# Performance work log

Measured on AMD Instinct MI355X. Metric: run time of the kernel, lower is better.

The kernel has to match this reference:

```python
import jax, jax.numpy as jnp
import numpy as np

F, V, NF, T = 240, 100000, 16, 2048


def _mesh_normalize(v):
    # v: (B, N, 3)
    mmax = jnp.max(v, axis=1, keepdims=True)
    mmin = jnp.min(v, axis=1, keepdims=True)
    v = v - (mmax + mmin) / 2
    big = jnp.max(v.reshape(v.shape[0], -1), axis=1)
    return v / big[:, None, None]


def _qmult(q1, q0):
    # Hamilton product, matches the torch qmult coefficient layout (wxyz)
    w0, x0, y0, z0 = q0[..., 0], q0[..., 1], q0[..., 2], q0[..., 3]
    w1, x1, y1, z1 = q1[..., 0], q1[..., 1], q1[..., 2], q1[..., 3]
    return jnp.stack([
        -x1 * x0 - y1 * y0 - z1 * z0 + w1 * w0,
         x1 * w0 + y1 * z0 - z1 * y0 + w1 * x0,
        -x1 * z0 + y1 * w0 + z1 * x0 + w1 * y0,
         x1 * y0 - y1 * x0 + z1 * w0 + w1 * z0], axis=-1)


def setup_inputs() -> dict:
    key = jax.random.key(0)
    k1, k2, k3, k4, k5 = jax.random.split(key, 5)
    # parameters initialized as in __init__ plus small perturbation (as after some training)
    tr = jnp.zeros((1, 1, F, 3)).at[0, 0, 0, 2].set(2.0) + 0.01 * jax.random.normal(k1, (1, 1, F, 3))
    q = jnp.zeros((1, F, 4)).at[:, :, 0].set(1.0) + 0.01 * jax.random.normal(k2, (1, F, 4))
    vp = 0.01 * jax.random.normal(k3, (1, V, 3))
    tex = jnp.ones((1, NF, T, T)) + 0.1 * jax.random.normal(k4, (1, NF, T, T))
    iv = _mesh_normalize(jax.random.normal(k5, (1, V, 3)))
    off = jnp.zeros((1, 1, F, 7)).at[:, :, :, 3].set(1.0)  # identity quaternion offsets, zero translation offsets
    of = jnp.arange(F, dtype=jnp.int32)
    return dict(translation_p=tr, quaternion_p=q, vertices_p=vp, texture_map=tex,
                ivertices=iv, offsets=off, opt_frames=of)


def reference(translation_p, quaternion_p, vertices_p, texture_map, ivertices, offsets, opt_frames):
    # opt_frames == arange(F): every frame is optimized, so no detach branch fires
    # and the per-frame python loop vectorizes (no cross-frame data dependence in outputs).
    qf = quaternion_p[0]                                      # (F, 4)
    qn = qf / jnp.linalg.norm(qf, axis=-1, keepdims=True)
    offq = offsets[0, 0, :, 3:]                               # (F, 4)
    offn = offq / jnp.linalg.norm(offq, axis=-1, keepdims=True)
    qprod = _qmult(qn, offn)                                  # (F, 4)
    # frame 0 uses the bare normalized quaternion; frames >=1 include the offset product
    q_all = jnp.concatenate([qn[:1], qprod[1:]], axis=0)      # (F, 4)
    t_all = jnp.concatenate(
        [translation_p[:, :, :1], translation_p[:, :, 1:] + offsets[:, :, 1:, :3]], axis=2)  # (1,1,F,3)

    of = opt_frames
    w = (of - jnp.concatenate([of[:1], of[:-1]])).astype(t_all.dtype)  # (K,)

    # tdiff = wghts * comp_tran_diff(translation[0,0,opt_frames])
    t = t_all[0, 0][of]                                       # (K, 3)
    vd = jnp.abs(t[1:] - t[:-1])
    vd = jnp.where(vd < 0.2, jnp.zeros_like(vd), vd)
    vd = jnp.concatenate([jnp.zeros_like(vd[:1]), vd], axis=0)
    tdiff = w * jnp.linalg.norm(vd, axis=1)

    # qdiff: first entry is qdist(quaternion0, quaternion0) with quaternion0 = last-loop value
    qlast = q_all[-1]
    d0 = 1.0 - jnp.sum(qlast * qlast) ** 2
    qa = q_all[of[1:] - 1]
    qb = q_all[of[1:]]
    kd = 1.0 - jnp.sum(qa * qb, axis=-1) ** 2
    qdiff = w * jnp.concatenate([d0[None], kd], axis=0)

    # predict_vertices=True, mesh_normalize=True
    vertices = _mesh_normalize(ivertices + vertices_p)

    # features == 'deep' -> raw texture map (no sigmoid)
    return (t_all[:, :, of], q_all[None][:, of], vertices, texture_map, tdiff, qdiff)
```

## Files before the change

kernel.cpp:

```cpp
#include <hip/hip_runtime.h>
#include <float.h>
#include <math.h>

#define F_MAX 512
#define RED_BLOCKS 32
#define COPY_GRID 1024

typedef float f4 __attribute__((ext_vector_type(4)));

__global__ __launch_bounds__(256) void minmax_frames_kernel(
    const f4* __restrict__ iv4, const f4* __restrict__ vp4, int nv4,
    float* __restrict__ partial,
    const float* __restrict__ tr,
    const float* __restrict__ q,
    const float* __restrict__ off,
    const int*   __restrict__ of,
    float* __restrict__ out_t,
    float* __restrict__ out_q,
    float* __restrict__ out_td,
    float* __restrict__ out_qd,
    int F)
{
    const int t = threadIdx.x;

    if (blockIdx.x != 0) {
        float mx0=-FLT_MAX, mx1=-FLT_MAX, mx2=-FLT_MAX;
        float mn0= FLT_MAX, mn1= FLT_MAX, mn2= FLT_MAX;
        const int gstride = (gridDim.x - 1) * blockDim.x;
        for (int i = (blockIdx.x - 1) * blockDim.x + t; i < nv4; i += gstride) {
            f4 a = iv4[i] + vp4[i];
            switch (i % 3) {
            case 0:
                mx0=fmaxf(mx0,a[0]); mn0=fminf(mn0,a[0]);
                mx1=fmaxf(mx1,a[1]); mn1=fminf(mn1,a[1]);
                mx2=fmaxf(mx2,a[2]); mn2=fminf(mn2,a[2]);
                mx0=fmaxf(mx0,a[3]); mn0=fminf(mn0,a[3]);
                break;
            case 1:
                mx1=fmaxf(mx1,a[0]); mn1=fminf(mn1,a[0]);
                mx2=fmaxf(mx2,a[1]); mn2=fminf(mn2,a[1]);
                mx0=fmaxf(mx0,a[2]); mn0=fminf(mn0,a[2]);
                mx1=fmaxf(mx1,a[3]); mn1=fminf(mn1,a[3]);
                break;
            default:
                mx2=fmaxf(mx2,a[0]); mn2=fminf(mn2,a[0]);
                mx0=fmaxf(mx0,a[1]); mn0=fminf(mn0,a[1]);
                mx1=fmaxf(mx1,a[2]); mn1=fminf(mn1,a[2]);
                mx2=fmaxf(mx2,a[3]); mn2=fminf(mn2,a[3]);
                break;
            }
        }
        __shared__ float s[256][6];
        s[t][0]=mx0; s[t][1]=mx1; s[t][2]=mx2; s[t][3]=mn0; s[t][4]=mn1; s[t][5]=mn2;
        __syncthreads();
        for (int w = 128; w >= 1; w >>= 1) {
            if (t < w) {
                s[t][0] = fmaxf(s[t][0], s[t+w][0]);
                s[t][1] = fmaxf(s[t][1], s[t+w][1]);
                s[t][2] = fmaxf(s[t][2], s[t+w][2]);
                s[t][3] = fminf(s[t][3], s[t+w][3]);
                s[t][4] = fminf(s[t][4], s[t+w][4]);
                s[t][5] = fminf(s[t][5], s[t+w][5]);
            }
            __syncthreads();
        }
        if (t == 0) {
            #pragma unroll
            for (int k = 0; k < 6; ++k)
                partial[(blockIdx.x - 1)*6 + k] = s[0][k];
        }
        return;
    }

    __shared__ float qall[F_MAX][4];
    __shared__ float tall[F_MAX][3];

    for (int f = t; f < F; f += blockDim.x) {
        float w1 = q[4*f+0], x1 = q[4*f+1], y1 = q[4*f+2], z1 = q[4*f+3];
        float n1 = sqrtf(w1*w1 + x1*x1 + y1*y1 + z1*z1);
        w1 /= n1; x1 /= n1; y1 /= n1; z1 /= n1;
        float w0 = off[7*f+3], x0 = off[7*f+4], y0 = off[7*f+5], z0 = off[7*f+6];
        float n0 = sqrtf(w0*w0 + x0*x0 + y0*y0 + z0*z0);
        w0 /= n0; x0 /= n0; y0 /= n0; z0 /= n0;
        float pw = -x1*x0 - y1*y0 - z1*z0 + w1*w0;
        float px =  x1*w0 + y1*z0 - z1*y0 + w1*x0;
        float py = -x1*z0 + y1*w0 + z1*x0 + w1*y0;
        float pz =  x1*y0 - y1*x0 + z1*w0 + w1*z0;
        if (f == 0) { pw = w1; px = x1; py = y1; pz = z1; }
        qall[f][0] = pw; qall[f][1] = px; qall[f][2] = py; qall[f][3] = pz;
        float o0 = 0.f, o1 = 0.f, o2 = 0.f;
        if (f >= 1) { o0 = off[7*f+0]; o1 = off[7*f+1]; o2 = off[7*f+2]; }
        tall[f][0] = tr[3*f+0] + o0;
        tall[f][1] = tr[3*f+1] + o1;
        tall[f][2] = tr[3*f+2] + o2;
    }
    __syncthreads();

    for (int j = t; j < F; j += blockDim.x) {
        const int fj = of[j];
        out_t[3*j+0] = tall[fj][0];
        out_t[3*j+1] = tall[fj][1];
        out_t[3*j+2] = tall[fj][2];
        out_q[4*j+0] = qall[fj][0];
        out_q[4*j+1] = qall[fj][1];
        out_q[4*j+2] = qall[fj][2];
        out_q[4*j+3] = qall[fj][3];

        float wj = (j == 0) ? 0.0f : (float)(of[j] - of[j-1]);

        float td = 0.0f;
        if (j >= 1) {
            const int fp = of[j-1];
            float ssum = 0.0f;
            #pragma unroll
            for (int c = 0; c < 3; ++c) {
                float d = fabsf(tall[fj][c] - tall[fp][c]);
                if (d < 0.2f) d = 0.0f;
                ssum += d * d;
            }
            td = wj * sqrtf(ssum);
        }
        out_td[j] = td;

        float qd;
        if (j == 0) {
            float sm = qall[F-1][0]*qall[F-1][0] + qall[F-1][1]*qall[F-1][1]
                     + qall[F-1][2]*qall[F-1][2] + qall[F-1][3]*qall[F-1][3];
            qd = wj * (1.0f - sm*sm);
        } else {
            int ia = fj - 1;
            if (ia < 0) ia += F;
            float sm = qall[ia][0]*qall[fj][0] + qall[ia][1]*qall[fj][1]
                     + qall[ia][2]*qall[fj][2] + qall[ia][3]*qall[fj][3];
            qd = wj * (1.0f - sm*sm);
        }
        out_qd[j] = qd;
    }
}

__global__ __launch_bounds__(256) void copy_finalize_norm_kernel(
    const f4* __restrict__ tex, f4* __restrict__ out_tex, long n_tex4,
    const float* __restrict__ partial,
    const f4* __restrict__ iv4, const f4* __restrict__ vp4,
    f4* __restrict__ out_v, int nv4)
{
    const int t = threadIdx.x;
    const long nthreads = (long)gridDim.x * blockDim.x;

    for (long i = (long)blockIdx.x * blockDim.x + t; i < n_tex4; i += nthreads) {
        f4 v = __builtin_nontemporal_load(&tex[i]);
        out_tex[i] = v;
    }

    const int gvid = blockIdx.x * blockDim.x + t;
    if (gvid < nv4) {
        float mx0=-FLT_MAX, mx1=-FLT_MAX, mx2=-FLT_MAX;
        float mn0= FLT_MAX, mn1= FLT_MAX, mn2= FLT_MAX;
        #pragma unroll
        for (int b = 0; b < RED_BLOCKS; ++b) {
            mx0 = fmaxf(mx0, partial[6*b+0]);
            mx1 = fmaxf(mx1, partial[6*b+1]);
            mx2 = fmaxf(mx2, partial[6*b+2]);
            mn0 = fminf(mn0, partial[6*b+3]);
            mn1 = fminf(mn1, partial[6*b+4]);
            mn2 = fminf(mn2, partial[6*b+5]);
        }
        const float c0 = (mx0 + mn0) * 0.5f;
        const float c1 = (mx1 + mn1) * 0.5f;
        const float c2 = (mx2 + mn2) * 0.5f;
        const float big = fmaxf(fmaxf(mx0 - c0, mx1 - c1), mx2 - c2);

        f4 a = iv4[gvid] + vp4[gvid];
        f4 r;
        switch (gvid % 3) {
        case 0:
            r[0]=(a[0]-c0)/big; r[1]=(a[1]-c1)/big;
            r[2]=(a[2]-c2)/big; r[3]=(a[3]-c0)/big; break;
        case 1:
            r[0]=(a[0]-c1)/big; r[1]=(a[1]-c2)/big;
            r[2]=(a[2]-c0)/big; r[3]=(a[3]-c1)/big; break;
        default:
            r[0]=(a[0]-c2)/big; r[1]=(a[1]-c0)/big;
            r[2]=(a[2]-c1)/big; r[3]=(a[3]-c2)/big; break;
        }
        out_v[gvid] = r;
    }
}

extern "C" void kernel_launch(void* const* d_in, const int* in_sizes, int n_in,
                              void* d_out, int out_size, void* d_ws, size_t ws_size,
                              hipStream_t stream) {
    const float* tr  = (const float*)d_in[0];
    const float* q   = (const float*)d_in[1];
    const float* vp  = (const float*)d_in[2];
    const float* tex = (const float*)d_in[3];
    const float* iv  = (const float*)d_in[4];
    const float* off = (const float*)d_in[5];
    const int*   of  = (const int*)d_in[6];

    const int F    = in_sizes[6];
    const int nt   = in_sizes[0];
    const int nq   = in_sizes[1];
    const int nv   = in_sizes[2];
    const int ntex = in_sizes[3];

    float* out     = (float*)d_out;
    float* out_t   = out;
    float* out_q   = out + nt;
    float* out_v   = out + nt + nq;
    float* out_tex = out + nt + nq + nv;
    float* out_td  = out + (size_t)nt + nq + nv + ntex;
    float* out_qd  = out_td + F;

    float* partial = (float*)d_ws;

    const int nv4 = nv / 4;

    minmax_frames_kernel<<<RED_BLOCKS + 1, 256, 0, stream>>>(
        (const f4*)iv, (const f4*)vp, nv4, partial,
        tr, q, off, of, out_t, out_q, out_td, out_qd, F);

    const long n_tex4 = (long)ntex / 4;
    copy_finalize_norm_kernel<<<COPY_GRID, 256, 0, stream>>>(
        (const f4*)tex, (f4*)out_tex, n_tex4,
        partial, (const f4*)iv, (const f4*)vp, (f4*)out_v, nv4);
}
```

Measured before the change: 90.45 us.

## Fuse reduction and copy kernels into one launch with atomic flag handoff

Merges the min/max reduction kernel and the texture-copy/normalize kernel into a single launch. Blocks 1..32 publish partial reductions and bump a global counter with release semantics. The blocks that normalize vertices spin on that counter after finishing their texture copy. This removes one kernel launch and the serialization gap between them, but adds a memset and a spin-wait that depends on the reducer blocks being co-resident, which carries a deadlock risk if they are not scheduled.

```diff
diff --git a/kernel.cpp b/kernel.cpp
--- a/kernel.cpp
+++ b/kernel.cpp
@@ -8,9 +8,10 @@
 
 typedef float f4 __attribute__((ext_vector_type(4)));
 
-__global__ __launch_bounds__(256) void minmax_frames_kernel(
+__global__ __launch_bounds__(256) void fused_kernel(
+    const f4* __restrict__ tex, f4* __restrict__ out_tex, long n_tex4,
     const f4* __restrict__ iv4, const f4* __restrict__ vp4, int nv4,
-    float* __restrict__ partial,
+    float* __restrict__ partial, unsigned int* __restrict__ flag,
     const float* __restrict__ tr,
     const float* __restrict__ q,
     const float* __restrict__ off,
@@ -19,15 +20,17 @@
     float* __restrict__ out_q,
     float* __restrict__ out_td,
     float* __restrict__ out_qd,
+    f4* __restrict__ out_v,
     int F)
 {
     const int t = threadIdx.x;
-
-    if (blockIdx.x != 0) {
+    const int b = blockIdx.x;
+
+    if (b >= 1 && b <= RED_BLOCKS) {
         float mx0=-FLT_MAX, mx1=-FLT_MAX, mx2=-FLT_MAX;
         float mn0= FLT_MAX, mn1= FLT_MAX, mn2= FLT_MAX;
-        const int gstride = (gridDim.x - 1) * blockDim.x;
-        for (int i = (blockIdx.x - 1) * blockDim.x + t; i < nv4; i += gstride) {
+        const int gstride = RED_BLOCKS * 256;
+        for (int i = (b - 1) * 256 + t; i < nv4; i += gstride) {
             f4 a = iv4[i] + vp4[i];
             switch (i % 3) {
             case 0:
@@ -66,104 +69,98 @@
         }
         if (t == 0) {
             #pragma unroll
-            for (int k = 0; k < 6; ++k)
-                partial[(blockIdx.x - 1)*6 + k] = s[0][k];
-        }
-        return;
+            for (int k = 0; k < 6; ++k) partial[(b - 1)*6 + k] = s[0][k];
+            __hip_atomic_fetch_add(flag, 1u, __ATOMIC_RELEASE,
+                                   __HIP_MEMORY_SCOPE_AGENT);
+        }
+    } else if (b == 0) {
+        __shared__ float qall[F_MAX][4];
+        __shared__ float tall[F_MAX][3];
+
+        for (int f = t; f < F; f += blockDim.x) {
+            float w1 = q[4*f+0], x1 = q[4*f+1], y1 = q[4*f+2], z1 = q[4*f+3];
+            float n1 = sqrtf(w1*w1 + x1*x1 + y1*y1 + z1*z1);
+            w1 /= n1; x1 /= n1; y1 /= n1; z1 /= n1;
+            float w0 = off[7*f+3], x0 = off[7*f+4], y0 = off[7*f+5], z0 = off[7*f+6];
+            float n0 = sqrtf(w0*w0 + x0*x0 + y0*y0 + z0*z0);
+            w0 /= n0; x0 /= n0; y0 /= n0; z0 /= n0;
+            float pw = -x1*x0 - y1*y0 - z1*z0 + w1*w0;
+            float px =  x1*w0 + y1*z0 - z1*y0 + w1*x0;
+            float py = -x1*z0 + y1*w0 + z1*x0 + w1*y0;
+            float pz =  x1*y0 - y1*x0 + z1*w0 + w1*z0;
+            if (f == 0) { pw = w1; px = x1; py = y1; pz = z1; }
+            qall[f][0] = pw; qall[f][1] = px; qall[f][2] = py; qall[f][3] = pz;
+            float o0 = 0.f, o1 = 0.f, o2 = 0.f;
+            if (f >= 1) { o0 = off[7*f+0]; o1 = off[7*f+1]; o2 = off[7*f+2]; }
+            tall[f][0] = tr[3*f+0] + o0;
+            tall[f][1] = tr[3*f+1] + o1;
+            tall[f][2] = tr[3*f+2] + o2;
+        }
+        __syncthreads();
+
+        for (int j = t; j < F; j += blockDim.x) {
+            const int fj = of[j];
+            out_t[3*j+0] = tall[fj][0];
+            out_t[3*j+1] = tall[fj][1];
+            out_t[3*j+2] = tall[fj][2];
+            out_q[4*j+0] = qall[fj][0];
+            out_q[4*j+1] = qall[fj][1];
+            out_q[4*j+2] = qall[fj][2];
+            out_q[4*j+3] = qall[fj][3];
+
+            float wj = (j == 0) ? 0.0f : (float)(of[j] - of[j-1]);
+
+            float td = 0.0f;
+            if (j >= 1) {
+                const int fp = of[j-1];
+                float ssum = 0.0f;
+                #pragma unroll
+                for (int c = 0; c < 3; ++c) {
+                    float d = fabsf(tall[fj][c] - tall[fp][c]);
+                    if (d < 0.2f) d = 0.0f;
+                    ssum += d * d;
+                }
+                td = wj * sqrtf(ssum);
+            }
+            out_td[j] = td;
+
+            float qd;
+            if (j == 0) {
+                float sm = qall[F-1][0]*qall[F-1][0] + qall[F-1][1]*qall[F-1][1]
+                         + qall[F-1][2]*qall[F-1][2] + qall[F-1][3]*qall[F-1][3];
+                qd = wj * (1.0f - sm*sm);
+            } else {
+                int ia = fj - 1;
+                if (ia < 0) ia += F;
+                float sm = qall[ia][0]*qall[fj][0] + qall[ia][1]*qall[fj][1]
+                         + qall[ia][2]*qall[fj][2] + qall[ia][3]*qall[fj][3];
+                qd = wj * (1.0f - sm*sm);
+            }
+            out_qd[j] = qd;
+        }
     }
 
-    __shared__ float qall[F_MAX][4];
-    __shared__ float tall[F_MAX][3];
-
-    for (int f = t; f < F; f += blockDim.x) {
-        float w1 = q[4*f+0], x1 = q[4*f+1], y1 = q[4*f+2], z1 = q[4*f+3];
-        float n1 = sqrtf(w1*w1 + x1*x1 + y1*y1 + z1*z1);
-        w1 /= n1; x1 /= n1; y1 /= n1; z1 /= n1;
-        float w0 = off[7*f+3], x0 = off[7*f+4], y0 = off[7*f+5], z0 = off[7*f+6];
-        float n0 = sqrtf(w0*w0 + x0*x0 + y0*y0 + z0*z0);
-        w0 /= n0; x0 /= n0; y0 /= n0; z0 /= n0;
-        float pw = -x1*x0 - y1*y0 - z1*z0 + w1*w0;
-        float px =  x1*w0 + y1*z0 - z1*y0 + w1*x0;
-        float py = -x1*z0 + y1*w0 + z1*x0 + w1*y0;
-        float pz =  x1*y0 - y1*x0 + z1*w0 + w1*z0;
-        if (f == 0) { pw = w1; px = x1; py = y1; pz = z1; }
-        qall[f][0] = pw; qall[f][1] = px; qall[f][2] = py; qall[f][3] = pz;
-        float o0 = 0.f, o1 = 0.f, o2 = 0.f;
-        if (f >= 1) { o0 = off[7*f+0]; o1 = off[7*f+1]; o2 = off[7*f+2]; }
-        tall[f][0] = tr[3*f+0] + o0;
-        tall[f][1] = tr[3*f+1] + o1;
-        tall[f][2] = tr[3*f+2] + o2;
-    }
-    __syncthreads();
-
-    for (int j = t; j < F; j += blockDim.x) {
-        const int fj = of[j];
-        out_t[3*j+0] = tall[fj][0];
-        out_t[3*j+1] = tall[fj][1];
-        out_t[3*j+2] = tall[fj][2];
-        out_q[4*j+0] = qall[fj][0];
-        out_q[4*j+1] = qall[fj][1];
-        out_q[4*j+2] = qall[fj][2];
-        out_q[4*j+3] = qall[fj][3];
-
-        float wj = (j == 0) ? 0.0f : (float)(of[j] - of[j-1]);
-
-        float td = 0.0f;
-        if (j >= 1) {
-            const int fp = of[j-1];
-            float ssum = 0.0f;
-            #pragma unroll
-            for (int c = 0; c < 3; ++c) {
-                float d = fabsf(tall[fj][c] - tall[fp][c]);
-                if (d < 0.2f) d = 0.0f;
-                ssum += d * d;
-            }
-            td = wj * sqrtf(ssum);
-        }
-        out_td[j] = td;
-
-        float qd;
-        if (j == 0) {
-            float sm = qall[F-1][0]*qall[F-1][0] + qall[F-1][1]*qall[F-1][1]
-                     + qall[F-1][2]*qall[F-1][2] + qall[F-1][3]*qall[F-1][3];
-            qd = wj * (1.0f - sm*sm);
-        } else {
-            int ia = fj - 1;
-            if (ia < 0) ia += F;
-            float sm = qall[ia][0]*qall[fj][0] + qall[ia][1]*qall[fj][1]
-                     + qall[ia][2]*qall[fj][2] + qall[ia][3]*qall[fj][3];
-            qd = wj * (1.0f - sm*sm);
-        }
-        out_qd[j] = qd;
-    }
-}
-
-__global__ __launch_bounds__(256) void copy_finalize_norm_kernel(
-    const f4* __restrict__ tex, f4* __restrict__ out_tex, long n_tex4,
-    const float* __restrict__ partial,
-    const f4* __restrict__ iv4, const f4* __restrict__ vp4,
-    f4* __restrict__ out_v, int nv4)
-{
-    const int t = threadIdx.x;
     const long nthreads = (long)gridDim.x * blockDim.x;
-
-    for (long i = (long)blockIdx.x * blockDim.x + t; i < n_tex4; i += nthreads) {
+    for (long i = (long)b * blockDim.x + t; i < n_tex4; i += nthreads) {
         f4 v = __builtin_nontemporal_load(&tex[i]);
         out_tex[i] = v;
     }
 
-    const int gvid = blockIdx.x * blockDim.x + t;
+    const int gvid = b * (int)blockDim.x + t;
     if (gvid < nv4) {
+        while (__hip_atomic_load(flag, __ATOMIC_ACQUIRE,
+                                 __HIP_MEMORY_SCOPE_AGENT) < RED_BLOCKS) { }
+
         float mx0=-FLT_MAX, mx1=-FLT_MAX, mx2=-FLT_MAX;
         float mn0= FLT_MAX, mn1= FLT_MAX, mn2= FLT_MAX;
         #pragma unroll
-        for (int b = 0; b < RED_BLOCKS; ++b) {
-            mx0 = fmaxf(mx0, partial[6*b+0]);
-            mx1 = fmaxf(mx1, partial[6*b+1]);
-            mx2 = fmaxf(mx2, partial[6*b+2]);
-            mn0 = fminf(mn0, partial[6*b+3]);
-            mn1 = fminf(mn1, partial[6*b+4]);
-            mn2 = fminf(mn2, partial[6*b+5]);
+        for (int p = 0; p < RED_BLOCKS; ++p) {
+            mx0 = fmaxf(mx0, partial[6*p+0]);
+            mx1 = fmaxf(mx1, partial[6*p+1]);
+            mx2 = fmaxf(mx2, partial[6*p+2]);
+            mn0 = fminf(mn0, partial[6*p+3]);
+            mn1 = fminf(mn1, partial[6*p+4]);
+            mn2 = fminf(mn2, partial[6*p+5]);
         }
         const float c0 = (mx0 + mn0) * 0.5f;
         const float c1 = (mx1 + mn1) * 0.5f;
@@ -212,16 +209,18 @@
     float* out_td  = out + (size_t)nt + nq + nv + ntex;
     float* out_qd  = out_td + F;
 
-    float* partial = (float*)d_ws;
-
-    const int nv4 = nv / 4;
-
-    minmax_frames_kernel<<<RED_BLOCKS + 1, 256, 0, stream>>>(
-        (const f4*)iv, (const f4*)vp, nv4, partial,
-        tr, q, off, of, out_t, out_q, out_td, out_qd, F);
-
+    float*        partial = (float*)d_ws;
+    unsigned int* flag    = (unsigned int*)((char*)d_ws + RED_BLOCKS*6*sizeof(float));
+
+    hipMemsetAsync(flag, 0, sizeof(unsigned int), stream);
+
+    const int  nv4    = nv / 4;
     const long n_tex4 = (long)ntex / 4;
-    copy_finalize_norm_kernel<<<COPY_GRID, 256, 0, stream>>>(
+
+    fused_kernel<<<COPY_GRID, 256, 0, stream>>>(
         (const f4*)tex, (f4*)out_tex, n_tex4,
-        partial, (const f4*)iv, (const f4*)vp, (f4*)out_v, nv4);
+        (const f4*)iv, (const f4*)vp, nv4,
+        partial, flag,
+        tr, q, off, of, out_t, out_q, out_td, out_qd,
+        (f4*)out_v, F);
 }
```

Measured after the change: 101.0 us. +11.7%, slower.
